# Performance work log

Hardware: AMD Instinct MI355X
Metric: run time of the kernel (lower is better)

## Reference

```python
import jax, jax.numpy as jnp
import numpy as np
import math

N = 100000   # outputSize (memory bank rows)
D = 128      # inputSize (feature dim)
B = 128      # batch size
K = 4096     # number of negatives per sample
T = 0.07     # temperature
MOMENTUM = 0.5


def setup_inputs() -> dict:
    key = jax.random.key(0)
    k1, k2, k3, k4, k5 = jax.random.split(key, 5)
    stdv = 1.0 / math.sqrt(D / 3.0)
    # l2-normalized features, as produced by the encoder in contrastive setups
    v1 = jax.random.normal(k1, (B, D), dtype=jnp.float32)
    v1 = v1 / jnp.linalg.norm(v1, axis=1, keepdims=True)
    v2 = jax.random.normal(k2, (B, D), dtype=jnp.float32)
    v2 = v2 / jnp.linalg.norm(v2, axis=1, keepdims=True)
    idx = jax.random.randint(k3, (B, K + 1), 0, N, dtype=jnp.int32)  # pos+neg bank rows
    y = jnp.arange(B, dtype=jnp.int32)  # distinct positive slots (first-visit behavior)
    # memory buffers initialized U(-stdv, stdv), as in torch.rand*2*stdv - stdv
    memory_v1 = jax.random.uniform(k4, (N, D), dtype=jnp.float32, minval=-stdv, maxval=stdv)
    memory_v2 = jax.random.uniform(k5, (N, D), dtype=jnp.float32, minval=-stdv, maxval=stdv)
    return {"v1": v1, "v2": v2, "idx": idx, "y": y,
            "memory_v1": memory_v1, "memory_v2": memory_v2}


def reference(v1, v2, idx, y, memory_v1, memory_v2):
    n_out = memory_v1.shape[0]
    # gather K+1 rows per sample (detached in the original -> stop_gradient)
    w1 = jax.lax.stop_gradient(memory_v1[idx])  # [B, K+1, D]
    w2 = jax.lax.stop_gradient(memory_v2[idx])  # [B, K+1, D]
    # batched vector-matrix product + exp/T
    out_v2 = jnp.exp(jnp.einsum('bkd,bd->bk', w1, v2) / T)  # [B, K+1]
    out_v1 = jnp.exp(jnp.einsum('bkd,bd->bk', w2, v1) / T)  # [B, K+1]
    # normalization constants (first-call Z computation: mean * outputSize)
    Z_v1 = jax.lax.stop_gradient(out_v1.mean()) * n_out
    Z_v2 = jax.lax.stop_gradient(out_v2.mean()) * n_out
    out_v1 = out_v1 / Z_v1
    out_v2 = out_v2 / Z_v2
    # momentum-blended normalize-and-scatter memory update (no_grad in torch)
    upd1 = MOMENTUM * memory_v1[y] + (1.0 - MOMENTUM) * v1  # [B, D]
    upd1 = upd1 / jnp.linalg.norm(upd1, axis=1, keepdims=True)
    new_memory_v1 = memory_v1.at[y].set(upd1)
    upd2 = MOMENTUM * memory_v2[y] + (1.0 - MOMENTUM) * v2
    upd2 = upd2 / jnp.linalg.norm(upd2, axis=1, keepdims=True)
    new_memory_v2 = memory_v2.at[y].set(upd2)
    return out_v1, out_v2, new_memory_v1, new_memory_v2
```

## Files before the change

### kernel.cpp

```cpp
#include <hip/hip_runtime.h>
#include <math.h>

constexpr int N_ROWS = 100000;
constexpr int D      = 128;
constexpr int B      = 128;
constexpr int KP1    = 4097;
constexpr int TOTAL_PAIRS = B * KP1;
constexpr float INV_T = 1.0f / 0.07f;
constexpr int N4 = N_ROWS * (D / 4);

constexpr int SC_BLOCKS = 1024;
constexpr int CP_BLOCKS = 1024;

__global__ void init_ws_kernel(float* ws) {
    if (threadIdx.x < 2) ws[threadIdx.x] = 0.0f;
}

__device__ __forceinline__ float dot4(float4 a, float4 b) {
    return a.x * b.x + a.y * b.y + a.z * b.z + a.w * b.w;
}

__device__ __forceinline__ float red32(float v) {
    #pragma unroll
    for (int off = 16; off >= 1; off >>= 1) v += __shfl_xor(v, off);
    return v;
}

__global__ __launch_bounds__(256) void mega_kernel(
    const float* __restrict__ v1, const float* __restrict__ v2,
    const int* __restrict__ idx,
    const float* __restrict__ mem1, const float* __restrict__ mem2,
    float* __restrict__ out,
    float* __restrict__ sums,
    float4* __restrict__ o1, float4* __restrict__ o2)
{
    if (blockIdx.x & 1) {
        int cid = blockIdx.x >> 1;
        const float4* __restrict__ m1 = (const float4*)mem1;
        const float4* __restrict__ m2 = (const float4*)mem2;
        int tid = cid * 256 + threadIdx.x;
        int stride = CP_BLOCKS * 256;
        for (int i = tid; i < N4; i += stride) {
            o1[i] = m1[i];
            o2[i] = m2[i];
        }
        return;
    }

    const int sid = blockIdx.x >> 1;
    const int l   = threadIdx.x & 31;
    const int grp = threadIdx.x >> 5;
    const int g   = sid * 8 + grp;
    const int b   = g >> 6;
    const int gk  = g & 63;

    const float4* __restrict__ m1 = (const float4*)mem1;
    const float4* __restrict__ m2 = (const float4*)mem2;
    const float4 a1 = ((const float4*)v1)[b * 32 + l];
    const float4 a2 = ((const float4*)v2)[b * 32 + l];
    const int base = b * KP1;

    float acc1 = 0.0f, acc2 = 0.0f;
    int k = gk;
    for (; k + 64 < KP1; k += 128) {
        int p0 = base + k, p1 = base + k + 64;
        int r0 = idx[p0], r1 = idx[p1];
        float4 w10 = m1[(size_t)r0 * 32 + l];
        float4 w20 = m2[(size_t)r0 * 32 + l];
        float4 w11 = m1[(size_t)r1 * 32 + l];
        float4 w21 = m2[(size_t)r1 * 32 + l];

        float d10 = red32(dot4(w20, a1));
        float d20 = red32(dot4(w10, a2));
        float d11 = red32(dot4(w21, a1));
        float d21 = red32(dot4(w11, a2));

        if (l == 0) {
            float e10 = __expf(d10 * INV_T);
            float e20 = __expf(d20 * INV_T);
            float e11 = __expf(d11 * INV_T);
            float e21 = __expf(d21 * INV_T);
            out[p0]               = e10;
            out[TOTAL_PAIRS + p0] = e20;
            out[p1]               = e11;
            out[TOTAL_PAIRS + p1] = e21;
            acc1 += e10 + e11;
            acc2 += e20 + e21;
        }
    }
    for (; k < KP1; k += 64) {
        int p0 = base + k;
        int r0 = idx[p0];
        float4 w10 = m1[(size_t)r0 * 32 + l];
        float4 w20 = m2[(size_t)r0 * 32 + l];
        float d10 = red32(dot4(w20, a1));
        float d20 = red32(dot4(w10, a2));
        if (l == 0) {
            float e10 = __expf(d10 * INV_T);
            float e20 = __expf(d20 * INV_T);
            out[p0]               = e10;
            out[TOTAL_PAIRS + p0] = e20;
            acc1 += e10;
            acc2 += e20;
        }
    }

    __shared__ float s1[8], s2[8];
    if (l == 0) { s1[grp] = acc1; s2[grp] = acc2; }
    __syncthreads();
    if (threadIdx.x == 0) {
        float t1 = 0.0f, t2 = 0.0f;
        #pragma unroll
        for (int i = 0; i < 8; ++i) { t1 += s1[i]; t2 += s2[i]; }
        atomicAdd(&sums[0], t1);
        atomicAdd(&sums[1], t2);
    }
}

__global__ __launch_bounds__(256) void finish_kernel(
    float* __restrict__ out, const float* __restrict__ sums,
    const float* __restrict__ v1, const float* __restrict__ v2,
    const int* __restrict__ y,
    const float* __restrict__ mem1, const float* __restrict__ mem2,
    float* __restrict__ o1, float* __restrict__ o2)
{
    if (blockIdx.x < 2 * B && threadIdx.x < 64) {
        int b    = blockIdx.x & (B - 1);
        int bank = blockIdx.x >> 7;
        int lane = threadIdx.x;
        const float2* __restrict__ m = (const float2*)(bank ? mem2 : mem1);
        const float2* __restrict__ v = (const float2*)(bank ? v2 : v1);
        float2* __restrict__ o       = (float2*)(bank ? o2 : o1);
        int row = y[b];
        float2 mv = m[(size_t)row * 64 + lane];
        float2 vv = v[b * 64 + lane];
        float2 u;
        u.x = 0.5f * mv.x + 0.5f * vv.x;
        u.y = 0.5f * mv.y + 0.5f * vv.y;
        float ss = u.x * u.x + u.y * u.y;
        #pragma unroll
        for (int off = 32; off >= 1; off >>= 1) ss += __shfl_xor(ss, off);
        float inv = 1.0f / sqrtf(ss);
        float2 r; r.x = u.x * inv; r.y = u.y * inv;
        o[(size_t)row * 64 + lane] = r;
    }

    float sc1 = (float)((double)TOTAL_PAIRS / ((double)sums[0] * (double)N_ROWS));
    float sc2 = (float)((double)TOTAL_PAIRS / ((double)sums[1] * (double)N_ROWS));
    int stride = gridDim.x * blockDim.x;
    for (int i = blockIdx.x * blockDim.x + threadIdx.x; i < 2 * TOTAL_PAIRS;
         i += stride) {
        out[i] *= (i < TOTAL_PAIRS) ? sc1 : sc2;
    }
}

extern "C" void kernel_launch(void* const* d_in, const int* in_sizes, int n_in,
                              void* d_out, int out_size, void* d_ws, size_t ws_size,
                              hipStream_t stream) {
    const float* v1   = (const float*)d_in[0];
    const float* v2   = (const float*)d_in[1];
    const int*   idx  = (const int*)d_in[2];
    const int*   y    = (const int*)d_in[3];
    const float* mem1 = (const float*)d_in[4];
    const float* mem2 = (const float*)d_in[5];

    float* out = (float*)d_out;
    float* out_mem1 = out + 2 * (size_t)TOTAL_PAIRS;
    float* out_mem2 = out_mem1 + (size_t)N_ROWS * D;
    float* sums = (float*)d_ws;

    init_ws_kernel<<<1, 64, 0, stream>>>(sums);

    mega_kernel<<<SC_BLOCKS + CP_BLOCKS, 256, 0, stream>>>(
        v1, v2, idx, mem1, mem2, out, sums,
        (float4*)out_mem1, (float4*)out_mem2);

    finish_kernel<<<1024, 256, 0, stream>>>(
        out, sums, v1, v2, y, mem1, mem2, out_mem1, out_mem2);
}
```

Before: 287.5 us.

## Compute each pair's dot products in a single thread instead of a 32-lane group

The gather-dot kernel changes from 32 lanes cooperating on one (b,k) pair, joined by shuffle reductions, to one thread computing a full 128-element dot product per pair with strided float4 loads. The block mix changes to two scoring blocks per copy block, with 2048 scoring blocks, and launch bounds ask for 4 blocks per CU. This removes the per-pair shuffle reductions and the single-lane exp and store. In exchange, each thread now walks a whole 512-byte row on its own, so loads are no longer coalesced across a wave: neighbouring lanes hit different random rows, which can hurt memory efficiency.

```diff
diff --git a/kernel.cpp b/kernel.cpp
--- a/kernel.cpp
+++ b/kernel.cpp
@@ -9,8 +9,9 @@
 constexpr float INV_T = 1.0f / 0.07f;
 constexpr int N4 = N_ROWS * (D / 4);
 
-constexpr int SC_BLOCKS = 1024;
-constexpr int CP_BLOCKS = 1024;
+constexpr int SCB = 2048;
+constexpr int CPB = 1024;
+constexpr int SC_THREADS = SCB * 256;
 
 __global__ void init_ws_kernel(float* ws) {
     if (threadIdx.x < 2) ws[threadIdx.x] = 0.0f;
@@ -20,13 +21,7 @@
     return a.x * b.x + a.y * b.y + a.z * b.z + a.w * b.w;
 }
 
-__device__ __forceinline__ float red32(float v) {
-    #pragma unroll
-    for (int off = 16; off >= 1; off >>= 1) v += __shfl_xor(v, off);
-    return v;
-}
-
-__global__ __launch_bounds__(256) void mega_kernel(
+__global__ __launch_bounds__(256, 4) void mega_kernel(
     const float* __restrict__ v1, const float* __restrict__ v2,
     const int* __restrict__ idx,
     const float* __restrict__ mem1, const float* __restrict__ mem2,
@@ -34,12 +29,15 @@
     float* __restrict__ sums,
     float4* __restrict__ o1, float4* __restrict__ o2)
 {
-    if (blockIdx.x & 1) {
-        int cid = blockIdx.x >> 1;
+    const unsigned bx = blockIdx.x;
+    const unsigned role = bx % 3u;
+
+    if (role == 0u) {
+        int cid = bx / 3u;
         const float4* __restrict__ m1 = (const float4*)mem1;
         const float4* __restrict__ m2 = (const float4*)mem2;
         int tid = cid * 256 + threadIdx.x;
-        int stride = CP_BLOCKS * 256;
+        int stride = CPB * 256;
         for (int i = tid; i < N4; i += stride) {
             o1[i] = m1[i];
             o2[i] = m2[i];
@@ -47,71 +45,55 @@
         return;
     }
 
-    const int sid = blockIdx.x >> 1;
-    const int l   = threadIdx.x & 31;
-    const int grp = threadIdx.x >> 5;
-    const int g   = sid * 8 + grp;
-    const int b   = g >> 6;
-    const int gk  = g & 63;
+    const int sid = (bx / 3u) * 2 + (role - 1);
+    const int tid = sid * 256 + threadIdx.x;
 
     const float4* __restrict__ m1 = (const float4*)mem1;
     const float4* __restrict__ m2 = (const float4*)mem2;
-    const float4 a1 = ((const float4*)v1)[b * 32 + l];
-    const float4 a2 = ((const float4*)v2)[b * 32 + l];
-    const int base = b * KP1;
+    const float4* __restrict__ vv1 = (const float4*)v1;
+    const float4* __restrict__ vv2 = (const float4*)v2;
 
     float acc1 = 0.0f, acc2 = 0.0f;
-    int k = gk;
-    for (; k + 64 < KP1; k += 128) {
-        int p0 = base + k, p1 = base + k + 64;
-        int r0 = idx[p0], r1 = idx[p1];
-        float4 w10 = m1[(size_t)r0 * 32 + l];
-        float4 w20 = m2[(size_t)r0 * 32 + l];
-        float4 w11 = m1[(size_t)r1 * 32 + l];
-        float4 w21 = m2[(size_t)r1 * 32 + l];
 
-        float d10 = red32(dot4(w20, a1));
-        float d20 = red32(dot4(w10, a2));
-        float d11 = red32(dot4(w21, a1));
-        float d21 = red32(dot4(w11, a2));
+    for (int p = tid; p < TOTAL_PAIRS; p += SC_THREADS) {
+        int b = (int)((unsigned)p / (unsigned)KP1);
+        int row = idx[p];
+        const float4* __restrict__ w1 = m1 + (size_t)row * 32;
+        const float4* __restrict__ w2 = m2 + (size_t)row * 32;
+        const float4* __restrict__ a1 = vv1 + b * 32;
+        const float4* __restrict__ a2 = vv2 + b * 32;
 
-        if (l == 0) {
-            float e10 = __expf(d10 * INV_T);
-            float e20 = __expf(d20 * INV_T);
-            float e11 = __expf(d11 * INV_T);
-            float e21 = __expf(d21 * INV_T);
-            out[p0]               = e10;
-            out[TOTAL_PAIRS + p0] = e20;
-            out[p1]               = e11;
-            out[TOTAL_PAIRS + p1] = e21;
-            acc1 += e10 + e11;
-            acc2 += e20 + e21;
+        float d1 = 0.0f, d2 = 0.0f;
+        #pragma unroll 8
+        for (int c = 0; c < 32; ++c) {
+            float4 x1 = w1[c];
+            float4 x2 = w2[c];
+            float4 y1 = a1[c];
+            float4 y2 = a2[c];
+            d1 += dot4(x2, y1);
+            d2 += dot4(x1, y2);
         }
-    }
-    for (; k < KP1; k += 64) {
-        int p0 = base + k;
-        int r0 = idx[p0];
-        float4 w10 = m1[(size_t)r0 * 32 + l];
-        float4 w20 = m2[(size_t)r0 * 32 + l];
-        float d10 = red32(dot4(w20, a1));
-        float d20 = red32(dot4(w10, a2));
-        if (l == 0) {
-            float e10 = __expf(d10 * INV_T);
-            float e20 = __expf(d20 * INV_T);
-            out[p0]               = e10;
-            out[TOTAL_PAIRS + p0] = e20;
-            acc1 += e10;
-            acc2 += e20;
-        }
+
+        float e1 = __expf(d1 * INV_T);
+        float e2 = __expf(d2 * INV_T);
+        out[p]               = e1;
+        out[TOTAL_PAIRS + p] = e2;
+        acc1 += e1;
+        acc2 += e2;
     }
 
-    __shared__ float s1[8], s2[8];
-    if (l == 0) { s1[grp] = acc1; s2[grp] = acc2; }
+    #pragma unroll
+    for (int off = 32; off >= 1; off >>= 1) {
+        acc1 += __shfl_xor(acc1, off);
+        acc2 += __shfl_xor(acc2, off);
+    }
+    __shared__ float s1[4], s2[4];
+    const int wave = threadIdx.x >> 6;
+    if ((threadIdx.x & 63) == 0) { s1[wave] = acc1; s2[wave] = acc2; }
     __syncthreads();
     if (threadIdx.x == 0) {
-        float t1 = 0.0f, t2 = 0.0f;
-        #pragma unroll
-        for (int i = 0; i < 8; ++i) { t1 += s1[i]; t2 += s2[i]; }
+        float t1 = s1[0] + s1[1] + s1[2] + s1[3];
+        float t2 = s2[0] + s2[1] + s2[2] + s2[3];
         atomicAdd(&sums[0], t1);
         atomicAdd(&sums[1], t2);
     }
@@ -171,7 +153,7 @@
 
     init_ws_kernel<<<1, 64, 0, stream>>>(sums);
 
-    mega_kernel<<<SC_BLOCKS + CP_BLOCKS, 256, 0, stream>>>(
+    mega_kernel<<<SCB + CPB, 256, 0, stream>>>(
         v1, v2, idx, mem1, mem2, out, sums,
         (float4*)out_mem1, (float4*)out_mem2);
 
```

After: 399.4 us. 38.9% more time.
